# Performance work log

Measured on AMD Instinct MI355X. Metric: run time of the kernel, lower is better.

## Reference

```python
import jax, jax.numpy as jnp
import numpy as np

B, N, C, D, O = 32, 512, 16, 256, 256


def setup_inputs() -> dict:
    key = jax.random.key(0)
    k1, k2, k3, k4, k5, k6 = jax.random.split(key, 6)
    std = 1.0 / np.sqrt(D)
    nodes = jax.random.normal(k1, (B, N, D), jnp.float32)
    children = jax.random.randint(k2, (B, N, C), 0, N)  # 0 == no-child sentinel
    w_t = jax.random.normal(k3, (D, O), jnp.float32) * std
    w_l = jax.random.normal(k4, (D, O), jnp.float32) * std
    w_r = jax.random.normal(k5, (D, O), jnp.float32) * std
    conv = jax.random.normal(k6, (O,), jnp.float32) * np.sqrt(2.0 / D)
    return {"nodes": nodes, "w_t": w_t, "w_l": w_l, "w_r": w_r, "conv": conv,
            "children": children}


def _coefs(children):
    # children: (B, N, C) int. Returns coef (B, N, C+1, 3) = stack(c_t, c_r, c_l).
    b, n, c = children.shape
    y = c + 1
    has_child = jnp.minimum(children, 1).astype(jnp.float32)          # (B,N,C)
    mask = jnp.concatenate([jnp.zeros((b, n, 1), jnp.float32), has_child], axis=2)  # (B,N,Y)
    # eta_t: 1 at slot 0 (parent), 0 elsewhere
    c_t = jnp.concatenate([jnp.ones((b, n, 1), jnp.float32),
                           jnp.zeros((b, n, c), jnp.float32)], axis=2)
    # eta_r
    ns = jnp.count_nonzero(children, axis=2).astype(jnp.float32)[..., None]  # (B,N,1)
    p = jnp.arange(-1.0, c, dtype=jnp.float32)                        # (Y,): -1,0,1,...
    child_idx = p * mask                                              # (B,N,Y)
    singles = (jnp.arange(y) == 1).astype(jnp.float32) * 0.5          # (Y,)
    denom = jnp.where(ns == 1.0, 1.0, ns - 1.0)                       # safe divide
    c_r = jnp.where(ns == 1.0,
                    jnp.broadcast_to(singles, mask.shape),
                    (1.0 - c_t) * (child_idx / denom))
    # eta_l
    c_l = (1.0 - c_t) * (1.0 - c_r) * mask
    return jnp.stack([c_t, c_r, c_l], axis=3)                         # (B,N,Y,3)


def reference(nodes, w_t, w_l, w_r, conv, children):
    b, n, d = nodes.shape
    c = children.shape[2]
    # gather children embeddings: child_emb[b,i,j] = nodes[b, children[b,i,j]]
    flat_idx = children.reshape(b, n * c)
    child_emb = jnp.take_along_axis(nodes, flat_idx[:, :, None], axis=1)
    child_emb = child_emb.reshape(b, n, c, d)
    child_emb = jnp.where((children == 0)[..., None], 0.0, child_emb)
    tree = jnp.concatenate([nodes[:, :, None, :], child_emb], axis=2)  # (B,N,Y,D)
    coef = _coefs(children)                                            # (B,N,Y,3)
    weights = jnp.stack([w_t, w_r, w_l], axis=0)                       # (3,D,O)
    agg = jnp.einsum('bnyd,bnyk->bnkd', tree, coef)                    # (B,N,3,D)
    res = jnp.einsum('bnkd,kdo->bno', agg, weights)                    # (B,N,O)
    return jax.nn.leaky_relu(res + conv, negative_slope=0.01)
```

## Files before the change

kernel.cpp:

```cpp
#include <hip/hip_runtime.h>
#include <hip/hip_bf16.h>
#include <stdint.h>

#define CC 16
#define OO 256
#define NSLAB 24
#define AGG_ELS (16384 * 768)

typedef __attribute__((ext_vector_type(8))) short bf16x8;
typedef __attribute__((ext_vector_type(4))) float f32x4;

__device__ __forceinline__ unsigned short f2bf(float x) {
    unsigned u = __builtin_bit_cast(unsigned, x);
    u += 0x7FFFu + ((u >> 16) & 1u);
    return (unsigned short)(u >> 16);
}

__device__ __forceinline__ void cp16(const void* g, void* l) {
    __builtin_amdgcn_global_load_lds(
        (const __attribute__((address_space(1))) unsigned int*)g,
        (__attribute__((address_space(3))) unsigned int*)l, 16, 0, 0);
}

__global__ __launch_bounds__(256) void prep(
    const float* __restrict__ nodes, const float* __restrict__ wt,
    const float* __restrict__ wrp, const float* __restrict__ wl,
    unsigned short* __restrict__ agg, unsigned short* __restrict__ wsb) {

    __shared__ unsigned short T[256 * 40];
    const int p = blockIdx.x;
    const int tid = threadIdx.x;

    if (p < 2048) {
        const int pp = (p & 7) * 256 + (p >> 3);
        const size_t t = (size_t)pp * 256 + tid;
        const float4* s = (const float4*)nodes + t * 2;
        float4 a = s[0], b = s[1];
        uint4 u;
        u.x = (unsigned)f2bf(a.x) | ((unsigned)f2bf(a.y) << 16);
        u.y = (unsigned)f2bf(a.z) | ((unsigned)f2bf(a.w) << 16);
        u.z = (unsigned)f2bf(b.x) | ((unsigned)f2bf(b.y) << 16);
        u.w = (unsigned)f2bf(b.z) | ((unsigned)f2bf(b.w) << 16);
        const size_t row = t >> 5;
        *(uint4*)(agg + row * 768 + (t & 31) * 8) = u;
        return;
    }
    const int slab = p - 2048;
    const int n = tid;
#pragma unroll
    for (int kk = 0; kk < 32; ++kk) {
        const int k = slab * 32 + kk;
        const float* s = (k < 256) ? wt : ((k < 512) ? wrp : wl);
        T[n * 40 + kk] = f2bf(s[(k & 255) * OO + n]);
    }
    __syncthreads();
    uint4* dst = (uint4*)(wsb + slab * 8192 + n * 32);
    const uint4* src = (const uint4*)&T[n * 40];
#pragma unroll
    for (int q = 0; q < 4; ++q) dst[q] = src[q];
}

__global__ __launch_bounds__(256, 8) void gather(
    const int* __restrict__ children, unsigned short* __restrict__ agg) {

    const int wave = threadIdx.x >> 6;
    const int lane = threadIdx.x & 63;
    const int p = blockIdx.x;
    const int g = (p & 7) * 512 + (p >> 3);
    const int nf = __builtin_amdgcn_readfirstlane(g * 4 + wave);
    const int brow = nf & ~511;

    const int* chp = children + (nf << 4);
    int cj[CC];
#pragma unroll
    for (int j = 0; j < CC; ++j) cj[j] = chp[j];
    int ns = 0;
#pragma unroll
    for (int j = 0; j < CC; ++j) ns += (cj[j] != 0) ? 1 : 0;
    const float inv_den = (ns > 1) ? 1.0f / (float)(ns - 1) : 0.0f;
    const bool single = (ns == 1);

    uint2 ec[CC];
#pragma unroll
    for (int j = 0; j < CC; ++j)
        ec[j] = *(const uint2*)(agg + (size_t)(brow + cj[j]) * 768 + lane * 4);

    float4 ar = make_float4(0.f, 0.f, 0.f, 0.f);
    float4 as = make_float4(0.f, 0.f, 0.f, 0.f);
#pragma unroll
    for (int j = 0; j < CC; ++j) {
        const float hasf = (cj[j] != 0) ? 1.0f : 0.0f;
        const float crr = single ? ((j == 0) ? 0.5f : 0.0f) : (float)j * inv_den;
        const float cr = crr * hasf;
        const float e0 = __builtin_bit_cast(float, ec[j].x << 16);
        const float e1 = __builtin_bit_cast(float, ec[j].x & 0xFFFF0000u);
        const float e2 = __builtin_bit_cast(float, ec[j].y << 16);
        const float e3 = __builtin_bit_cast(float, ec[j].y & 0xFFFF0000u);
        ar.x += cr * e0;   ar.y += cr * e1;   ar.z += cr * e2;   ar.w += cr * e3;
        as.x += hasf * e0; as.y += hasf * e1; as.z += hasf * e2; as.w += hasf * e3;
    }
    const float4 al = make_float4(as.x - ar.x, as.y - ar.y,
                                  as.z - ar.z, as.w - ar.w);

    unsigned short* rowp = agg + (size_t)nf * 768;
    uint2 u;
    u.x = (unsigned)f2bf(ar.x) | ((unsigned)f2bf(ar.y) << 16);
    u.y = (unsigned)f2bf(ar.z) | ((unsigned)f2bf(ar.w) << 16);
    *(uint2*)(rowp + 256 + lane * 4) = u;
    u.x = (unsigned)f2bf(al.x) | ((unsigned)f2bf(al.y) << 16);
    u.y = (unsigned)f2bf(al.z) | ((unsigned)f2bf(al.w) << 16);
    *(uint2*)(rowp + 512 + lane * 4) = u;
}

__global__ __launch_bounds__(256, 2) void gemm_ep(
    const unsigned short* __restrict__ agg, const unsigned short* __restrict__ wsb,
    const float* __restrict__ conv, float* __restrict__ out) {

    __shared__ unsigned short Ab[2][2048];
    __shared__ unsigned short Bb[2][4096];

    const int tid  = threadIdx.x;
    const int wave = tid >> 6;
    const int lane = tid & 63;
    const int quad = lane >> 4;
    const int l16  = lane & 15;
    const int x = blockIdx.x & 7;
    const int q = blockIdx.x >> 3;
    const int mtile = x * 32 + (q >> 1);
    const int ntile = q & 1;
    const int wrr = wave >> 1;
    const int wcc = wave & 1;

    const char* aggb = (const char*)agg + (size_t)mtile * (64 * 1536);
    const char* wsbb = (const char*)wsb + ntile * 8192;
    const int toff  = tid * 16;
    const int wbase = (tid & ~63) * 16;
    const char* arow = aggb + (size_t)(tid >> 2) * 1536 + (tid & 3) * 16;

    f32x4 acc[2][4];
#pragma unroll
    for (int mi = 0; mi < 2; ++mi)
#pragma unroll
        for (int ni = 0; ni < 4; ++ni)
            acc[mi][ni] = (f32x4){0.f, 0.f, 0.f, 0.f};

    auto stage = [&](int s, int b) {
        cp16(arow + s * 64, (char*)&Ab[b][0] + wbase);
        const char* gb = wsbb + s * 16384 + toff;
        cp16(gb,        (char*)&Bb[b][0] + wbase);
        cp16(gb + 4096, (char*)&Bb[b][0] + wbase + 4096);
    };

    stage(0, 0);
#pragma unroll 1
    for (int s = 0; s < NSLAB; ++s) {
        const int cur = s & 1;
        __syncthreads();
        if (s + 1 < NSLAB) stage(s + 1, cur ^ 1);

        bf16x8 af[2], bfr[4];
#pragma unroll
        for (int mi = 0; mi < 2; ++mi)
            af[mi] = *(const bf16x8*)&Ab[cur][(wrr * 32 + mi * 16 + l16) * 32 + quad * 8];
#pragma unroll
        for (int ni = 0; ni < 4; ++ni)
            bfr[ni] = *(const bf16x8*)&Bb[cur][(wcc * 64 + ni * 16 + l16) * 32 + quad * 8];
#pragma unroll
        for (int mi = 0; mi < 2; ++mi)
#pragma unroll
            for (int ni = 0; ni < 4; ++ni)
                acc[mi][ni] = __builtin_amdgcn_mfma_f32_16x16x32_bf16(
                    af[mi], bfr[ni], acc[mi][ni], 0, 0, 0);
    }

#pragma unroll
    for (int ni = 0; ni < 4; ++ni) {
        const int col = ntile * 128 + wcc * 64 + ni * 16 + l16;
        const float cv = conv[col];
#pragma unroll
        for (int mi = 0; mi < 2; ++mi) {
#pragma unroll
            for (int r = 0; r < 4; ++r) {
                const int row = mtile * 64 + wrr * 32 + mi * 16 + quad * 4 + r;
                float v = acc[mi][ni][r] + cv;
                v = (v > 0.f) ? v : 0.01f * v;
                out[(size_t)row * OO + col] = v;
            }
        }
    }
}

extern "C" void kernel_launch(void* const* d_in, const int* in_sizes, int n_in,
                              void* d_out, int out_size, void* d_ws, size_t ws_size,
                              hipStream_t stream) {
    const float* nodes    = (const float*)d_in[0];
    const float* w_t      = (const float*)d_in[1];
    const float* w_l      = (const float*)d_in[2];
    const float* w_r      = (const float*)d_in[3];
    const float* conv     = (const float*)d_in[4];
    const int*   children = (const int*)d_in[5];

    unsigned short* agg = (unsigned short*)d_ws;
    unsigned short* wsb = agg + AGG_ELS;

    prep<<<2048 + 24, 256, 0, stream>>>(nodes, w_t, w_r, w_l, agg, wsb);
    gather<<<4096, 256, 0, stream>>>(children, agg);
    gemm_ep<<<512, 256, 0, stream>>>(agg, wsb, conv, (float*)d_out);
}
```

Baseline: 110.3 us.

## Fuse prep, gather and GEMM into one persistent kernel with grid barriers

Replaces the three kernel launches with a single 512-block kernel that converts nodes and weights, performs the child gather, and runs the GEMM epilogue, separated by two atomic-counter grid barriers. The barrier counter is reset with a memset before each launch. The GEMM stage also drops LDS double buffering and loads MFMA operands directly from global memory. The aim is to remove launch gaps and inter-kernel drain. In exchange, each block must now do 8 gather rows sequentially, and the grid barrier only works if all 512 blocks are resident at the same time.

New measurement: 356.9 us. 3.24x slower.

```diff
diff --git a/kernel.cpp b/kernel.cpp
--- a/kernel.cpp
+++ b/kernel.cpp
@@ -6,6 +6,7 @@
 #define OO 256
 #define NSLAB 24
 #define AGG_ELS (16384 * 768)
+#define NBLK 512
 
 typedef __attribute__((ext_vector_type(8))) short bf16x8;
 typedef __attribute__((ext_vector_type(4))) float f32x4;
@@ -16,126 +17,123 @@
     return (unsigned short)(u >> 16);
 }
 
-__device__ __forceinline__ void cp16(const void* g, void* l) {
-    __builtin_amdgcn_global_load_lds(
-        (const __attribute__((address_space(1))) unsigned int*)g,
-        (__attribute__((address_space(3))) unsigned int*)l, 16, 0, 0);
+__device__ __forceinline__ void gbar(unsigned* c) {
+    __threadfence();
+    __syncthreads();
+    if (threadIdx.x == 0) {
+        __hip_atomic_fetch_add(c, 1u, __ATOMIC_ACQ_REL, __HIP_MEMORY_SCOPE_AGENT);
+        while (__hip_atomic_load(c, __ATOMIC_ACQUIRE, __HIP_MEMORY_SCOPE_AGENT) < NBLK)
+            __builtin_amdgcn_s_sleep(2);
+    }
+    __syncthreads();
+    __threadfence();
 }
 
-__global__ __launch_bounds__(256) void prep(
+__global__ __launch_bounds__(256, 2) void tbcnn_fused(
     const float* __restrict__ nodes, const float* __restrict__ wt,
     const float* __restrict__ wrp, const float* __restrict__ wl,
-    unsigned short* __restrict__ agg, unsigned short* __restrict__ wsb) {
+    const float* __restrict__ conv, const int* __restrict__ children,
+    unsigned short* __restrict__ agg, unsigned short* __restrict__ wsb,
+    unsigned* __restrict__ bar, float* __restrict__ out) {
 
     __shared__ unsigned short T[256 * 40];
-    const int p = blockIdx.x;
+
+    const int p   = blockIdx.x;
     const int tid = threadIdx.x;
+    const int x   = p & 7;
+    const int q   = p >> 3;
 
-    if (p < 2048) {
-        const int pp = (p & 7) * 256 + (p >> 3);
-        const size_t t = (size_t)pp * 256 + tid;
-        const float4* s = (const float4*)nodes + t * 2;
+    if (p < 24) {
+        const int slab = p;
+        const int n = tid;
+#pragma unroll
+        for (int kk = 0; kk < 32; ++kk) {
+            const int k = slab * 32 + kk;
+            const float* s = (k < 256) ? wt : ((k < 512) ? wrp : wl);
+            T[n * 40 + kk] = f2bf(s[(k & 255) * OO + n]);
+        }
+        __syncthreads();
+        uint4* dst = (uint4*)(wsb + slab * 8192 + n * 32);
+        const uint4* src = (const uint4*)&T[n * 40];
+#pragma unroll
+        for (int u = 0; u < 4; ++u) dst[u] = src[u];
+    }
+    const int rowbase = x * 2048 + q * 32;
+#pragma unroll
+    for (int u = 0; u < 4; ++u) {
+        const int unit = u * 256 + tid;
+        const int r  = rowbase + (unit >> 5);
+        const int ch = unit & 31;
+        const float4* s = (const float4*)(nodes + (size_t)r * 256 + ch * 8);
         float4 a = s[0], b = s[1];
-        uint4 u;
-        u.x = (unsigned)f2bf(a.x) | ((unsigned)f2bf(a.y) << 16);
-        u.y = (unsigned)f2bf(a.z) | ((unsigned)f2bf(a.w) << 16);
-        u.z = (unsigned)f2bf(b.x) | ((unsigned)f2bf(b.y) << 16);
-        u.w = (unsigned)f2bf(b.z) | ((unsigned)f2bf(b.w) << 16);
-        const size_t row = t >> 5;
-        *(uint4*)(agg + row * 768 + (t & 31) * 8) = u;
-        return;
+        uint4 v;
+        v.x = (unsigned)f2bf(a.x) | ((unsigned)f2bf(a.y) << 16);
+        v.y = (unsigned)f2bf(a.z) | ((unsigned)f2bf(a.w) << 16);
+        v.z = (unsigned)f2bf(b.x) | ((unsigned)f2bf(b.y) << 16);
+        v.w = (unsigned)f2bf(b.z) | ((unsigned)f2bf(b.w) << 16);
+        *(uint4*)(agg + (size_t)r * 768 + ch * 8) = v;
     }
-    const int slab = p - 2048;
-    const int n = tid;
-#pragma unroll
-    for (int kk = 0; kk < 32; ++kk) {
-        const int k = slab * 32 + kk;
-        const float* s = (k < 256) ? wt : ((k < 512) ? wrp : wl);
-        T[n * 40 + kk] = f2bf(s[(k & 255) * OO + n]);
-    }
-    __syncthreads();
-    uint4* dst = (uint4*)(wsb + slab * 8192 + n * 32);
-    const uint4* src = (const uint4*)&T[n * 40];
-#pragma unroll
-    for (int q = 0; q < 4; ++q) dst[q] = src[q];
-}
 
-__global__ __launch_bounds__(256, 8) void gather(
-    const int* __restrict__ children, unsigned short* __restrict__ agg) {
+    gbar(bar);
 
-    const int wave = threadIdx.x >> 6;
-    const int lane = threadIdx.x & 63;
-    const int p = blockIdx.x;
-    const int g = (p & 7) * 512 + (p >> 3);
-    const int nf = __builtin_amdgcn_readfirstlane(g * 4 + wave);
-    const int brow = nf & ~511;
-
-    const int* chp = children + (nf << 4);
-    int cj[CC];
-#pragma unroll
-    for (int j = 0; j < CC; ++j) cj[j] = chp[j];
-    int ns = 0;
-#pragma unroll
-    for (int j = 0; j < CC; ++j) ns += (cj[j] != 0) ? 1 : 0;
-    const float inv_den = (ns > 1) ? 1.0f / (float)(ns - 1) : 0.0f;
-    const bool single = (ns == 1);
-
-    uint2 ec[CC];
-#pragma unroll
-    for (int j = 0; j < CC; ++j)
-        ec[j] = *(const uint2*)(agg + (size_t)(brow + cj[j]) * 768 + lane * 4);
-
-    float4 ar = make_float4(0.f, 0.f, 0.f, 0.f);
-    float4 as = make_float4(0.f, 0.f, 0.f, 0.f);
-#pragma unroll
-    for (int j = 0; j < CC; ++j) {
-        const float hasf = (cj[j] != 0) ? 1.0f : 0.0f;
-        const float crr = single ? ((j == 0) ? 0.5f : 0.0f) : (float)j * inv_den;
-        const float cr = crr * hasf;
-        const float e0 = __builtin_bit_cast(float, ec[j].x << 16);
-        const float e1 = __builtin_bit_cast(float, ec[j].x & 0xFFFF0000u);
-        const float e2 = __builtin_bit_cast(float, ec[j].y << 16);
-        const float e3 = __builtin_bit_cast(float, ec[j].y & 0xFFFF0000u);
-        ar.x += cr * e0;   ar.y += cr * e1;   ar.z += cr * e2;   ar.w += cr * e3;
-        as.x += hasf * e0; as.y += hasf * e1; as.z += hasf * e2; as.w += hasf * e3;
-    }
-    const float4 al = make_float4(as.x - ar.x, as.y - ar.y,
-                                  as.z - ar.z, as.w - ar.w);
-
-    unsigned short* rowp = agg + (size_t)nf * 768;
-    uint2 u;
-    u.x = (unsigned)f2bf(ar.x) | ((unsigned)f2bf(ar.y) << 16);
-    u.y = (unsigned)f2bf(ar.z) | ((unsigned)f2bf(ar.w) << 16);
-    *(uint2*)(rowp + 256 + lane * 4) = u;
-    u.x = (unsigned)f2bf(al.x) | ((unsigned)f2bf(al.y) << 16);
-    u.y = (unsigned)f2bf(al.z) | ((unsigned)f2bf(al.w) << 16);
-    *(uint2*)(rowp + 512 + lane * 4) = u;
-}
-
-__global__ __launch_bounds__(256, 2) void gemm_ep(
-    const unsigned short* __restrict__ agg, const unsigned short* __restrict__ wsb,
-    const float* __restrict__ conv, float* __restrict__ out) {
-
-    __shared__ unsigned short Ab[2][2048];
-    __shared__ unsigned short Bb[2][4096];
-
-    const int tid  = threadIdx.x;
     const int wave = tid >> 6;
     const int lane = tid & 63;
-    const int quad = lane >> 4;
-    const int l16  = lane & 15;
-    const int x = blockIdx.x & 7;
-    const int q = blockIdx.x >> 3;
+    const int nbase = x * 2048 + q * 32 + wave * 8;
+#pragma unroll 2
+    for (int i = 0; i < 8; ++i) {
+        const int nf = __builtin_amdgcn_readfirstlane(nbase + i);
+        const int brow = nf & ~511;
+        const int* chp = children + (nf << 4);
+        int cj[CC];
+#pragma unroll
+        for (int j = 0; j < CC; ++j) cj[j] = chp[j];
+        int ns = 0;
+#pragma unroll
+        for (int j = 0; j < CC; ++j) ns += (cj[j] != 0) ? 1 : 0;
+        const float inv_den = (ns > 1) ? 1.0f / (float)(ns - 1) : 0.0f;
+        const bool single = (ns == 1);
+
+        uint2 ec[CC];
+#pragma unroll
+        for (int j = 0; j < CC; ++j)
+            ec[j] = *(const uint2*)(agg + (size_t)(brow + cj[j]) * 768 + lane * 4);
+
+        float4 ar = make_float4(0.f, 0.f, 0.f, 0.f);
+        float4 as = make_float4(0.f, 0.f, 0.f, 0.f);
+#pragma unroll
+        for (int j = 0; j < CC; ++j) {
+            const float hasf = (cj[j] != 0) ? 1.0f : 0.0f;
+            const float crr = single ? ((j == 0) ? 0.5f : 0.0f)
+                                     : (float)j * inv_den;
+            const float cr = crr * hasf;
+            const float e0 = __builtin_bit_cast(float, ec[j].x << 16);
+            const float e1 = __builtin_bit_cast(float, ec[j].x & 0xFFFF0000u);
+            const float e2 = __builtin_bit_cast(float, ec[j].y << 16);
+            const float e3 = __builtin_bit_cast(float, ec[j].y & 0xFFFF0000u);
+            ar.x += cr * e0;   ar.y += cr * e1;   ar.z += cr * e2;   ar.w += cr * e3;
+            as.x += hasf * e0; as.y += hasf * e1; as.z += hasf * e2; as.w += hasf * e3;
+        }
+        unsigned short* rowp = agg + (size_t)nf * 768;
+        uint2 v;
+        v.x = (unsigned)f2bf(ar.x) | ((unsigned)f2bf(ar.y) << 16);
+        v.y = (unsigned)f2bf(ar.z) | ((unsigned)f2bf(ar.w) << 16);
+        *(uint2*)(rowp + 256 + lane * 4) = v;
+        v.x = (unsigned)f2bf(as.x - ar.x) | ((unsigned)f2bf(as.y - ar.y) << 16);
+        v.y = (unsigned)f2bf(as.z - ar.z) | ((unsigned)f2bf(as.w - ar.w) << 16);
+        *(uint2*)(rowp + 512 + lane * 4) = v;
+    }
+
+    gbar(bar + 64);
+
     const int mtile = x * 32 + (q >> 1);
     const int ntile = q & 1;
     const int wrr = wave >> 1;
     const int wcc = wave & 1;
+    const int quad = lane >> 4;
+    const int l16  = lane & 15;
 
-    const char* aggb = (const char*)agg + (size_t)mtile * (64 * 1536);
-    const char* wsbb = (const char*)wsb + ntile * 8192;
-    const int toff  = tid * 16;
-    const int wbase = (tid & ~63) * 16;
-    const char* arow = aggb + (size_t)(tid >> 2) * 1536 + (tid & 3) * 16;
+    const unsigned short* aggA = agg + (size_t)mtile * 64 * 768;
+    const unsigned short* wsN  = wsb + (ntile * 128 + wcc * 64) * 32;
 
     f32x4 acc[2][4];
 #pragma unroll
@@ -144,33 +142,24 @@
         for (int ni = 0; ni < 4; ++ni)
             acc[mi][ni] = (f32x4){0.f, 0.f, 0.f, 0.f};
 
-    auto stage = [&](int s, int b) {
-        cp16(arow + s * 64, (char*)&Ab[b][0] + wbase);
-        const char* gb = wsbb + s * 16384 + toff;
-        cp16(gb,        (char*)&Bb[b][0] + wbase);
-        cp16(gb + 4096, (char*)&Bb[b][0] + wbase + 4096);
-    };
+    const unsigned short* aA0 = aggA + (size_t)(wrr * 32 + l16) * 768 + quad * 8;
+    const unsigned short* aA1 = aA0 + 16 * 768;
+    const unsigned short* aB  = wsN + (size_t)l16 * 32 + quad * 8;
 
-    stage(0, 0);
-#pragma unroll 1
+#pragma unroll 4
     for (int s = 0; s < NSLAB; ++s) {
-        const int cur = s & 1;
-        __syncthreads();
-        if (s + 1 < NSLAB) stage(s + 1, cur ^ 1);
-
-        bf16x8 af[2], bfr[4];
-#pragma unroll
-        for (int mi = 0; mi < 2; ++mi)
-            af[mi] = *(const bf16x8*)&Ab[cur][(wrr * 32 + mi * 16 + l16) * 32 + quad * 8];
+        bf16x8 af[2], bf[4];
+        af[0] = *(const bf16x8*)(aA0 + s * 32);
+        af[1] = *(const bf16x8*)(aA1 + s * 32);
 #pragma unroll
         for (int ni = 0; ni < 4; ++ni)
-            bfr[ni] = *(const bf16x8*)&Bb[cur][(wcc * 64 + ni * 16 + l16) * 32 + quad * 8];
+            bf[ni] = *(const bf16x8*)(aB + s * 8192 + ni * 16 * 32);
 #pragma unroll
         for (int mi = 0; mi < 2; ++mi)
 #pragma unroll
             for (int ni = 0; ni < 4; ++ni)
                 acc[mi][ni] = __builtin_amdgcn_mfma_f32_16x16x32_bf16(
-                    af[mi], bfr[ni], acc[mi][ni], 0, 0, 0);
+                    af[mi], bf[ni], acc[mi][ni], 0, 0, 0);
     }
 
 #pragma unroll
@@ -202,8 +191,9 @@
 
     unsigned short* agg = (unsigned short*)d_ws;
     unsigned short* wsb = agg + AGG_ELS;
+    unsigned* bar = (unsigned*)((char*)d_ws + (size_t)AGG_ELS * 2 + 768 * 256 * 2);
 
-    prep<<<2048 + 24, 256, 0, stream>>>(nodes, w_t, w_r, w_l, agg, wsb);
-    gather<<<4096, 256, 0, stream>>>(children, agg);
-    gemm_ep<<<512, 256, 0, stream>>>(agg, wsb, conv, (float*)d_out);
+    hipMemsetAsync(bar, 0, 512, stream);
+    tbcnn_fused<<<NBLK, 256, 0, stream>>>(nodes, w_t, w_r, w_l, conv, children,
+                                          agg, wsb, bar, (float*)d_out);
 }
```

## Fuse child gather-aggregation into GEMM, keeping aggregates in LDS

Applied to the files above, without the earlier changes.

Merges the gather kernel into the GEMM kernel. Each block of 32 rows computes the right and left child aggregates into shared memory, then runs the GEMM over all 256 output columns. The parent part of the A operand is read straight from the bf16 node buffer in global memory, and the weights are read directly from global memory without the LDS double-buffering. This removes one launch and the 768-wide intermediate round trip through global memory. The cost is that the gather phase cannot overlap with MFMA work, and the unstaged global loads for A and B may stall the matrix cores.

Result: no change. 108.8 us (-1.4%).

```diff
diff --git a/kernel.cpp b/kernel.cpp
--- a/kernel.cpp
+++ b/kernel.cpp
@@ -5,7 +5,8 @@
 #define CC 16
 #define OO 256
 #define NSLAB 24
-#define AGG_ELS (16384 * 768)
+#define NB_ELS (16384 * 256)
+#define A2STR 520
 
 typedef __attribute__((ext_vector_type(8))) short bf16x8;
 typedef __attribute__((ext_vector_type(4))) float f32x4;
@@ -16,16 +17,10 @@
     return (unsigned short)(u >> 16);
 }
 
-__device__ __forceinline__ void cp16(const void* g, void* l) {
-    __builtin_amdgcn_global_load_lds(
-        (const __attribute__((address_space(1))) unsigned int*)g,
-        (__attribute__((address_space(3))) unsigned int*)l, 16, 0, 0);
-}
-
 __global__ __launch_bounds__(256) void prep(
     const float* __restrict__ nodes, const float* __restrict__ wt,
     const float* __restrict__ wrp, const float* __restrict__ wl,
-    unsigned short* __restrict__ agg, unsigned short* __restrict__ wsb) {
+    unsigned short* __restrict__ nb, unsigned short* __restrict__ wsb) {
 
     __shared__ unsigned short T[256 * 40];
     const int p = blockIdx.x;
@@ -41,8 +36,7 @@
         u.y = (unsigned)f2bf(a.z) | ((unsigned)f2bf(a.w) << 16);
         u.z = (unsigned)f2bf(b.x) | ((unsigned)f2bf(b.y) << 16);
         u.w = (unsigned)f2bf(b.z) | ((unsigned)f2bf(b.w) << 16);
-        const size_t row = t >> 5;
-        *(uint4*)(agg + row * 768 + (t & 31) * 8) = u;
+        *(uint4*)(nb + (t >> 5) * 256 + (t & 31) * 8) = u;
         return;
     }
     const int slab = p - 2048;
@@ -60,83 +54,68 @@
     for (int q = 0; q < 4; ++q) dst[q] = src[q];
 }
 
-__global__ __launch_bounds__(256, 8) void gather(
-    const int* __restrict__ children, unsigned short* __restrict__ agg) {
+__global__ __launch_bounds__(256, 2) void tbcnn_fused(
+    const int* __restrict__ children, const unsigned short* __restrict__ nb,
+    const unsigned short* __restrict__ wsb, const float* __restrict__ conv,
+    float* __restrict__ out) {
 
-    const int wave = threadIdx.x >> 6;
-    const int lane = threadIdx.x & 63;
-    const int p = blockIdx.x;
-    const int g = (p & 7) * 512 + (p >> 3);
-    const int nf = __builtin_amdgcn_readfirstlane(g * 4 + wave);
-    const int brow = nf & ~511;
-
-    const int* chp = children + (nf << 4);
-    int cj[CC];
-#pragma unroll
-    for (int j = 0; j < CC; ++j) cj[j] = chp[j];
-    int ns = 0;
-#pragma unroll
-    for (int j = 0; j < CC; ++j) ns += (cj[j] != 0) ? 1 : 0;
-    const float inv_den = (ns > 1) ? 1.0f / (float)(ns - 1) : 0.0f;
-    const bool single = (ns == 1);
-
-    uint2 ec[CC];
-#pragma unroll
-    for (int j = 0; j < CC; ++j)
-        ec[j] = *(const uint2*)(agg + (size_t)(brow + cj[j]) * 768 + lane * 4);
-
-    float4 ar = make_float4(0.f, 0.f, 0.f, 0.f);
-    float4 as = make_float4(0.f, 0.f, 0.f, 0.f);
-#pragma unroll
-    for (int j = 0; j < CC; ++j) {
-        const float hasf = (cj[j] != 0) ? 1.0f : 0.0f;
-        const float crr = single ? ((j == 0) ? 0.5f : 0.0f) : (float)j * inv_den;
-        const float cr = crr * hasf;
-        const float e0 = __builtin_bit_cast(float, ec[j].x << 16);
-        const float e1 = __builtin_bit_cast(float, ec[j].x & 0xFFFF0000u);
-        const float e2 = __builtin_bit_cast(float, ec[j].y << 16);
-        const float e3 = __builtin_bit_cast(float, ec[j].y & 0xFFFF0000u);
-        ar.x += cr * e0;   ar.y += cr * e1;   ar.z += cr * e2;   ar.w += cr * e3;
-        as.x += hasf * e0; as.y += hasf * e1; as.z += hasf * e2; as.w += hasf * e3;
-    }
-    const float4 al = make_float4(as.x - ar.x, as.y - ar.y,
-                                  as.z - ar.z, as.w - ar.w);
-
-    unsigned short* rowp = agg + (size_t)nf * 768;
-    uint2 u;
-    u.x = (unsigned)f2bf(ar.x) | ((unsigned)f2bf(ar.y) << 16);
-    u.y = (unsigned)f2bf(ar.z) | ((unsigned)f2bf(ar.w) << 16);
-    *(uint2*)(rowp + 256 + lane * 4) = u;
-    u.x = (unsigned)f2bf(al.x) | ((unsigned)f2bf(al.y) << 16);
-    u.y = (unsigned)f2bf(al.z) | ((unsigned)f2bf(al.w) << 16);
-    *(uint2*)(rowp + 512 + lane * 4) = u;
-}
-
-__global__ __launch_bounds__(256, 2) void gemm_ep(
-    const unsigned short* __restrict__ agg, const unsigned short* __restrict__ wsb,
-    const float* __restrict__ conv, float* __restrict__ out) {
-
-    __shared__ unsigned short Ab[2][2048];
-    __shared__ unsigned short Bb[2][4096];
+    __shared__ unsigned short A2[32 * A2STR];
 
     const int tid  = threadIdx.x;
     const int wave = tid >> 6;
     const int lane = tid & 63;
+    const int x = blockIdx.x & 7;
+    const int q = blockIdx.x >> 3;
+    const int rbase = x * 2048 + q * 32;
+
+#pragma unroll 2
+    for (int i = 0; i < 8; ++i) {
+        const int m  = wave * 8 + i;
+        const int nf = __builtin_amdgcn_readfirstlane(rbase + m);
+        const int brow = nf & ~511;
+        const int* chp = children + (nf << 4);
+        int cj[CC];
+#pragma unroll
+        for (int j = 0; j < CC; ++j) cj[j] = chp[j];
+        int ns = 0;
+#pragma unroll
+        for (int j = 0; j < CC; ++j) ns += (cj[j] != 0) ? 1 : 0;
+        const float inv_den = (ns > 1) ? 1.0f / (float)(ns - 1) : 0.0f;
+        const bool single = (ns == 1);
+
+        uint2 ec[CC];
+#pragma unroll
+        for (int j = 0; j < CC; ++j)
+            ec[j] = *(const uint2*)(nb + (size_t)(brow + cj[j]) * 256 + lane * 4);
+
+        float4 ar = make_float4(0.f, 0.f, 0.f, 0.f);
+        float4 as = make_float4(0.f, 0.f, 0.f, 0.f);
+#pragma unroll
+        for (int j = 0; j < CC; ++j) {
+            const float hasf = (cj[j] != 0) ? 1.0f : 0.0f;
+            const float crr = single ? ((j == 0) ? 0.5f : 0.0f)
+                                     : (float)j * inv_den;
+            const float cr = crr * hasf;
+            const float e0 = __builtin_bit_cast(float, ec[j].x << 16);
+            const float e1 = __builtin_bit_cast(float, ec[j].x & 0xFFFF0000u);
+            const float e2 = __builtin_bit_cast(float, ec[j].y << 16);
+            const float e3 = __builtin_bit_cast(float, ec[j].y & 0xFFFF0000u);
+            ar.x += cr * e0;   ar.y += cr * e1;   ar.z += cr * e2;   ar.w += cr * e3;
+            as.x += hasf * e0; as.y += hasf * e1; as.z += hasf * e2; as.w += hasf * e3;
+        }
+        unsigned short* rowp = &A2[m * A2STR];
+        uint2 v;
+        v.x = (unsigned)f2bf(ar.x) | ((unsigned)f2bf(ar.y) << 16);
+        v.y = (unsigned)f2bf(ar.z) | ((unsigned)f2bf(ar.w) << 16);
+        *(uint2*)(rowp + lane * 4) = v;
+        v.x = (unsigned)f2bf(as.x - ar.x) | ((unsigned)f2bf(as.y - ar.y) << 16);
+        v.y = (unsigned)f2bf(as.z - ar.z) | ((unsigned)f2bf(as.w - ar.w) << 16);
+        *(uint2*)(rowp + 256 + lane * 4) = v;
+    }
+    __syncthreads();
+
     const int quad = lane >> 4;
     const int l16  = lane & 15;
-    const int x = blockIdx.x & 7;
-    const int q = blockIdx.x >> 3;
-    const int mtile = x * 32 + (q >> 1);
-    const int ntile = q & 1;
-    const int wrr = wave >> 1;
-    const int wcc = wave & 1;
-
-    const char* aggb = (const char*)agg + (size_t)mtile * (64 * 1536);
-    const char* wsbb = (const char*)wsb + ntile * 8192;
-    const int toff  = tid * 16;
-    const int wbase = (tid & ~63) * 16;
-    const char* arow = aggb + (size_t)(tid >> 2) * 1536 + (tid & 3) * 16;
-
     f32x4 acc[2][4];
 #pragma unroll
     for (int mi = 0; mi < 2; ++mi)
@@ -144,44 +123,50 @@
         for (int ni = 0; ni < 4; ++ni)
             acc[mi][ni] = (f32x4){0.f, 0.f, 0.f, 0.f};
 
-    auto stage = [&](int s, int b) {
-        cp16(arow + s * 64, (char*)&Ab[b][0] + wbase);
-        const char* gb = wsbb + s * 16384 + toff;
-        cp16(gb,        (char*)&Bb[b][0] + wbase);
-        cp16(gb + 4096, (char*)&Bb[b][0] + wbase + 4096);
-    };
+    const unsigned short* bbase = wsb + (wave * 64 + l16) * 32 + quad * 8;
+    const unsigned short* aG = nb + (size_t)(rbase + l16) * 256 + quad * 8;
+    const unsigned short* aL = &A2[l16 * A2STR + quad * 8];
 
-    stage(0, 0);
-#pragma unroll 1
-    for (int s = 0; s < NSLAB; ++s) {
-        const int cur = s & 1;
-        __syncthreads();
-        if (s + 1 < NSLAB) stage(s + 1, cur ^ 1);
-
-        bf16x8 af[2], bfr[4];
-#pragma unroll
-        for (int mi = 0; mi < 2; ++mi)
-            af[mi] = *(const bf16x8*)&Ab[cur][(wrr * 32 + mi * 16 + l16) * 32 + quad * 8];
+#pragma unroll 2
+    for (int s = 0; s < 8; ++s) {
+        bf16x8 af[2], bf[4];
+        af[0] = *(const bf16x8*)(aG + s * 32);
+        af[1] = *(const bf16x8*)(aG + 16 * 256 + s * 32);
 #pragma unroll
         for (int ni = 0; ni < 4; ++ni)
-            bfr[ni] = *(const bf16x8*)&Bb[cur][(wcc * 64 + ni * 16 + l16) * 32 + quad * 8];
+            bf[ni] = *(const bf16x8*)(bbase + s * 8192 + ni * 512);
 #pragma unroll
         for (int mi = 0; mi < 2; ++mi)
 #pragma unroll
             for (int ni = 0; ni < 4; ++ni)
                 acc[mi][ni] = __builtin_amdgcn_mfma_f32_16x16x32_bf16(
-                    af[mi], bfr[ni], acc[mi][ni], 0, 0, 0);
+                    af[mi], bf[ni], acc[mi][ni], 0, 0, 0);
+    }
+#pragma unroll 2
+    for (int s = 8; s < 24; ++s) {
+        bf16x8 af[2], bf[4];
+        af[0] = *(const bf16x8*)(aL + (s - 8) * 32);
+        af[1] = *(const bf16x8*)(aL + 16 * A2STR + (s - 8) * 32);
+#pragma unroll
+        for (int ni = 0; ni < 4; ++ni)
+            bf[ni] = *(const bf16x8*)(bbase + s * 8192 + ni * 512);
+#pragma unroll
+        for (int mi = 0; mi < 2; ++mi)
+#pragma unroll
+            for (int ni = 0; ni < 4; ++ni)
+                acc[mi][ni] = __builtin_amdgcn_mfma_f32_16x16x32_bf16(
+                    af[mi], bf[ni], acc[mi][ni], 0, 0, 0);
     }
 
 #pragma unroll
     for (int ni = 0; ni < 4; ++ni) {
-        const int col = ntile * 128 + wcc * 64 + ni * 16 + l16;
+        const int col = wave * 64 + ni * 16 + l16;
         const float cv = conv[col];
 #pragma unroll
         for (int mi = 0; mi < 2; ++mi) {
 #pragma unroll
             for (int r = 0; r < 4; ++r) {
-                const int row = mtile * 64 + wrr * 32 + mi * 16 + quad * 4 + r;
+                const int row = rbase + mi * 16 + quad * 4 + r;
                 float v = acc[mi][ni][r] + cv;
                 v = (v > 0.f) ? v : 0.01f * v;
                 out[(size_t)row * OO + col] = v;
@@ -200,10 +185,9 @@
     const float* conv     = (const float*)d_in[4];
     const int*   children = (const int*)d_in[5];
 
-    unsigned short* agg = (unsigned short*)d_ws;
-    unsigned short* wsb = agg + AGG_ELS;
+    unsigned short* nb  = (unsigned short*)d_ws;
+    unsigned short* wsb = nb + NB_ELS;
 
-    prep<<<2048 + 24, 256, 0, stream>>>(nodes, w_t, w_r, w_l, agg, wsb);
-    gather<<<4096, 256, 0, stream>>>(children, agg);
-    gemm_ep<<<512, 256, 0, stream>>>(agg, wsb, conv, (float*)d_out);
+    prep<<<2048 + 24, 256, 0, stream>>>(nodes, w_t, w_r, w_l, nb, wsb);
+    tbcnn_fused<<<512, 256, 0, stream>>>(children, nb, wsb, conv, (float*)d_out);
 }
```
